# Performance work log

Hardware: AMD Instinct MI355X
Metric: run time of the kernel (lower is better)

Reference implementation:

```python
import jax, jax.numpy as jnp
import numpy as np

B, C, T = 128, 64, 16384
RED = 16  # channels // reduction_ratio

def setup_inputs() -> dict:
    key = jax.random.key(0)
    k0, k1, k2 = jax.random.split(key, 3)
    x = jax.random.normal(k0, (B, C, T), dtype=jnp.float32)
    # torch Linear init ~ U(-1/sqrt(fan_in), 1/sqrt(fan_in)); scaled normals are fine for a reference
    w1 = jax.random.normal(k1, (RED, C), dtype=jnp.float32) / np.sqrt(C)
    b1 = jnp.zeros((RED,), dtype=jnp.float32)
    w2 = jax.random.normal(k2, (C, RED), dtype=jnp.float32) / np.sqrt(RED)
    b2 = jnp.zeros((C,), dtype=jnp.float32)
    return {"x": x, "w1": w1, "b1": b1, "w2": w2, "b2": b2}

def reference(x, w1, b1, w2, b2):
    # squeeze: global average pool over time -> [B, C]
    u = jnp.mean(x, axis=-1)
    # excitation: Linear -> ReLU -> Linear -> Sigmoid (torch Linear: y = u @ W.T + b)
    h = jax.nn.relu(jnp.einsum('bc,rc->br', u, w1) + b1)
    s = jax.nn.sigmoid(jnp.einsum('br,cr->bc', h, w2) + b2)
    # channel-wise rescale
    x_recal = x * s[:, :, None]
    return (x_recal, s)
```

## Files before the change

kernel.cpp:

```cpp
#include <hip/hip_runtime.h>

#define BB 128
#define CC 64
#define TT 16384
#define RED 16
#define ROWS (BB * CC)
#define T4 (TT / 4)
#define GB 16
#define NG (BB / GB)
#define ROWS_G (GB * CC)

typedef float f4 __attribute__((ext_vector_type(4)));

__global__ __launch_bounds__(256) void se_reduce(const f4* __restrict__ x,
                                                 float* __restrict__ u,
                                                 int rowBase) {
    const int row = rowBase + blockIdx.x;
    const int tid = threadIdx.x;
    const f4* xr = x + (size_t)row * T4;

    float sum = 0.f;
#pragma unroll
    for (int k = 0; k < T4 / 256; ++k) {
        f4 v = xr[tid + k * 256];
        sum += (v.x + v.y) + (v.z + v.w);
    }
#pragma unroll
    for (int off = 32; off > 0; off >>= 1)
        sum += __shfl_down(sum, off, 64);

    __shared__ float wsum[4];
    const int lane = tid & 63, wid = tid >> 6;
    if (lane == 0) wsum[wid] = sum;
    __syncthreads();
    if (tid == 0)
        u[row] = (wsum[0] + wsum[1] + wsum[2] + wsum[3]) * (1.0f / TT);
}

__global__ __launch_bounds__(256) void se_scale(const f4* __restrict__ x,
                                                const float* __restrict__ u,
                                                const float* __restrict__ w1,
                                                const float* __restrict__ b1,
                                                const float* __restrict__ w2,
                                                const float* __restrict__ b2,
                                                f4* __restrict__ out,
                                                float* __restrict__ s_out,
                                                int rowBase) {
    const int row = rowBase + blockIdx.x;
    const int b = row >> 6;
    const int c = row & (CC - 1);
    const int tid = threadIdx.x;
    __shared__ float s_sh;

    if (tid < 64) {
        const int r = tid & 15, q = tid >> 4;
        const float* ub  = u  + b * CC + q * 16;
        const float* w1p = w1 + r * CC + q * 16;
        float p = 0.f;
#pragma unroll
        for (int j = 0; j < 16; ++j) p = fmaf(ub[j], w1p[j], p);
        p += __shfl_xor(p, 16, 64);
        p += __shfl_xor(p, 32, 64);
        const float h = fmaxf(p + b1[r], 0.f);
        float prod = h * w2[c * RED + r];
        prod += __shfl_xor(prod, 1, 64);
        prod += __shfl_xor(prod, 2, 64);
        prod += __shfl_xor(prod, 4, 64);
        prod += __shfl_xor(prod, 8, 64);
        if (tid == 0) {
            const float sv = 1.0f / (1.0f + expf(-(prod + b2[c])));
            s_sh = sv;
            s_out[row] = sv;
        }
    }
    __syncthreads();
    const float sv = s_sh;

    const f4* xr = x + (size_t)row * T4;
    f4* orow = out + (size_t)row * T4;
#pragma unroll
    for (int k = 0; k < T4 / 256; ++k) {
        f4 v = xr[tid + k * 256];
        v.x *= sv; v.y *= sv; v.z *= sv; v.w *= sv;
        __builtin_nontemporal_store(v, &orow[tid + k * 256]);
    }
}

extern "C" void kernel_launch(void* const* d_in, const int* in_sizes, int n_in,
                              void* d_out, int out_size, void* d_ws, size_t ws_size,
                              hipStream_t stream) {
    const float* x  = (const float*)d_in[0];
    const float* w1 = (const float*)d_in[1];
    const float* b1 = (const float*)d_in[2];
    const float* w2 = (const float*)d_in[3];
    const float* b2 = (const float*)d_in[4];

    float* out   = (float*)d_out;
    float* s_out = out + (size_t)ROWS * TT;
    float* u_ws  = (float*)d_ws;

    for (int g = 0; g < NG; ++g) {
        se_reduce<<<ROWS_G, 256, 0, stream>>>((const f4*)x, u_ws, g * ROWS_G);
        se_scale<<<ROWS_G, 256, 0, stream>>>((const f4*)x, u_ws, w1, b1, w2, b2,
                                             (f4*)out, s_out, g * ROWS_G);
    }
}
```

Baseline: 276.4 us.

## Fuse reduce and scale into a cooperative persistent kernel with pipelined next-group reduction

Replaces the 16 alternating reduce/scale launches with a single cooperative kernel of 512 blocks, each handling two rows per group. While scaling the current group, each block also reads the next group's rows and accumulates their means, then synchronises the whole grid before the next group's MLP. The aim is to cut launch overhead and to overlap the reduction read with the scale pass while the data is still likely in cache. The cost is grid-wide barriers, and each pass now reads two rows at once. If the cooperative launch fails, a non-cooperative path runs instead that uses the same overlapped reduction.

```diff
diff --git a/kernel.cpp b/kernel.cpp
--- a/kernel.cpp
+++ b/kernel.cpp
@@ -1,4 +1,7 @@
 #include <hip/hip_runtime.h>
+#include <hip/hip_cooperative_groups.h>
+
+namespace cg = cooperative_groups;
 
 #define BB 128
 #define CC 64
@@ -9,99 +12,203 @@
 #define GB 16
 #define NG (BB / GB)
 #define ROWS_G (GB * CC)
+#define GRID_C 512
 
 typedef float f4 __attribute__((ext_vector_type(4)));
 
-__global__ __launch_bounds__(256) void se_reduce(const f4* __restrict__ x,
-                                                 float* __restrict__ u,
-                                                 int rowBase) {
-    const int row = rowBase + blockIdx.x;
+__device__ __forceinline__ float wave_mlp(const float* __restrict__ u,
+                                          const float* __restrict__ w1,
+                                          const float* __restrict__ b1,
+                                          const float* __restrict__ w2,
+                                          const float* __restrict__ b2,
+                                          int b, int c, int lane) {
+    const int r = lane & 15, q = lane >> 4;
+    const float* ub  = u  + b * CC + q * 16;
+    const float* w1p = w1 + r * CC + q * 16;
+    float p = 0.f;
+#pragma unroll
+    for (int j = 0; j < 16; ++j) p = fmaf(ub[j], w1p[j], p);
+    p += __shfl_xor(p, 16, 64);
+    p += __shfl_xor(p, 32, 64);
+    const float h = fmaxf(p + b1[r], 0.f);
+    float prod = h * w2[c * RED + r];
+    prod += __shfl_xor(prod, 1, 64);
+    prod += __shfl_xor(prod, 2, 64);
+    prod += __shfl_xor(prod, 4, 64);
+    prod += __shfl_xor(prod, 8, 64);
+    return 1.0f / (1.0f + expf(-(prod + b2[c])));
+}
+
+__global__ __launch_bounds__(256, 2) void se_fused(
+        const f4* __restrict__ x,
+        const float* __restrict__ w1, const float* __restrict__ b1,
+        const float* __restrict__ w2, const float* __restrict__ b2,
+        f4* __restrict__ out, float* __restrict__ s_out,
+        float* __restrict__ u) {
+    cg::grid_group grid = cg::this_grid();
+    const int i = blockIdx.x;
     const int tid = threadIdx.x;
+    const int lane = tid & 63, wid = tid >> 6;
+    __shared__ float wsum[2][4];
+    __shared__ float s_sh[2];
+
+#pragma unroll
+    for (int rr = 0; rr < 2; ++rr) {
+        const f4* xr = x + (size_t)(i + rr * GRID_C) * T4;
+        float sum = 0.f;
+#pragma unroll 4
+        for (int k = 0; k < T4 / 256; ++k) {
+            f4 v = xr[tid + k * 256];
+            sum += (v.x + v.y) + (v.z + v.w);
+        }
+#pragma unroll
+        for (int off = 32; off; off >>= 1) sum += __shfl_down(sum, off, 64);
+        if (lane == 0) wsum[rr][wid] = sum;
+        __syncthreads();
+    }
+    if (tid < 2)
+        u[i + tid * GRID_C] =
+            (wsum[tid][0] + wsum[tid][1] + wsum[tid][2] + wsum[tid][3]) * (1.0f / TT);
+    grid.sync();
+
+    for (int g = 0; g < NG; ++g) {
+        const int row0 = g * ROWS_G + i;
+        if (wid < 2) {
+            const int row = row0 + wid * GRID_C;
+            const float sv = wave_mlp(u, w1, b1, w2, b2, row >> 6, row & (CC - 1), lane);
+            if (lane == 0) { s_sh[wid] = sv; s_out[row] = sv; }
+        }
+        __syncthreads();
+
+#pragma unroll
+        for (int rr = 0; rr < 2; ++rr) {
+            const int row = row0 + rr * GRID_C;
+            const float sv = s_sh[rr];
+            const f4* xr = x + (size_t)row * T4;
+            f4* orw = out + (size_t)row * T4;
+            if (g + 1 < NG) {
+                const f4* xn = x + (size_t)(row + ROWS_G) * T4;
+                float sum = 0.f;
+#pragma unroll 4
+                for (int k = 0; k < T4 / 256; ++k) {
+                    f4 v = xr[tid + k * 256];
+                    f4 w = xn[tid + k * 256];
+                    v.x *= sv; v.y *= sv; v.z *= sv; v.w *= sv;
+                    __builtin_nontemporal_store(v, &orw[tid + k * 256]);
+                    sum += (w.x + w.y) + (w.z + w.w);
+                }
+#pragma unroll
+                for (int off = 32; off; off >>= 1) sum += __shfl_down(sum, off, 64);
+                if (lane == 0) wsum[rr][wid] = sum;
+            } else {
+#pragma unroll 4
+                for (int k = 0; k < T4 / 256; ++k) {
+                    f4 v = xr[tid + k * 256];
+                    v.x *= sv; v.y *= sv; v.z *= sv; v.w *= sv;
+                    __builtin_nontemporal_store(v, &orw[tid + k * 256]);
+                }
+            }
+        }
+        if (g + 1 < NG) {
+            __syncthreads();
+            if (tid < 2)
+                u[row0 + ROWS_G + tid * GRID_C] =
+                    (wsum[tid][0] + wsum[tid][1] + wsum[tid][2] + wsum[tid][3]) * (1.0f / TT);
+            grid.sync();
+        }
+    }
+}
+
+__global__ __launch_bounds__(256) void se_reduce0(const f4* __restrict__ x,
+                                                  float* __restrict__ u) {
+    const int row = blockIdx.x;
+    const int tid = threadIdx.x;
+    const int lane = tid & 63, wid = tid >> 6;
     const f4* xr = x + (size_t)row * T4;
-
     float sum = 0.f;
-#pragma unroll
+#pragma unroll 4
     for (int k = 0; k < T4 / 256; ++k) {
         f4 v = xr[tid + k * 256];
         sum += (v.x + v.y) + (v.z + v.w);
     }
 #pragma unroll
-    for (int off = 32; off > 0; off >>= 1)
-        sum += __shfl_down(sum, off, 64);
-
+    for (int off = 32; off; off >>= 1) sum += __shfl_down(sum, off, 64);
     __shared__ float wsum[4];
-    const int lane = tid & 63, wid = tid >> 6;
     if (lane == 0) wsum[wid] = sum;
     __syncthreads();
-    if (tid == 0)
-        u[row] = (wsum[0] + wsum[1] + wsum[2] + wsum[3]) * (1.0f / TT);
-}
-
-__global__ __launch_bounds__(256) void se_scale(const f4* __restrict__ x,
-                                                const float* __restrict__ u,
-                                                const float* __restrict__ w1,
-                                                const float* __restrict__ b1,
-                                                const float* __restrict__ w2,
-                                                const float* __restrict__ b2,
-                                                f4* __restrict__ out,
-                                                float* __restrict__ s_out,
-                                                int rowBase) {
-    const int row = rowBase + blockIdx.x;
-    const int b = row >> 6;
-    const int c = row & (CC - 1);
+    if (tid == 0) u[row] = (wsum[0] + wsum[1] + wsum[2] + wsum[3]) * (1.0f / TT);
+}
+
+__global__ __launch_bounds__(256) void se_phase(
+        const f4* __restrict__ x,
+        const float* __restrict__ w1, const float* __restrict__ b1,
+        const float* __restrict__ w2, const float* __restrict__ b2,
+        f4* __restrict__ out, float* __restrict__ s_out,
+        float* __restrict__ u, int g) {
+    const int row = g * ROWS_G + blockIdx.x;
     const int tid = threadIdx.x;
+    const int lane = tid & 63, wid = tid >> 6;
+    __shared__ float wsum[4];
     __shared__ float s_sh;
 
     if (tid < 64) {
-        const int r = tid & 15, q = tid >> 4;
-        const float* ub  = u  + b * CC + q * 16;
-        const float* w1p = w1 + r * CC + q * 16;
-        float p = 0.f;
-#pragma unroll
-        for (int j = 0; j < 16; ++j) p = fmaf(ub[j], w1p[j], p);
-        p += __shfl_xor(p, 16, 64);
-        p += __shfl_xor(p, 32, 64);
-        const float h = fmaxf(p + b1[r], 0.f);
-        float prod = h * w2[c * RED + r];
-        prod += __shfl_xor(prod, 1, 64);
-        prod += __shfl_xor(prod, 2, 64);
-        prod += __shfl_xor(prod, 4, 64);
-        prod += __shfl_xor(prod, 8, 64);
-        if (tid == 0) {
-            const float sv = 1.0f / (1.0f + expf(-(prod + b2[c])));
-            s_sh = sv;
-            s_out[row] = sv;
-        }
+        const float sv = wave_mlp(u, w1, b1, w2, b2, row >> 6, row & (CC - 1), lane);
+        if (lane == 0) { s_sh = sv; s_out[row] = sv; }
     }
     __syncthreads();
     const float sv = s_sh;
 
     const f4* xr = x + (size_t)row * T4;
-    f4* orow = out + (size_t)row * T4;
-#pragma unroll
-    for (int k = 0; k < T4 / 256; ++k) {
-        f4 v = xr[tid + k * 256];
-        v.x *= sv; v.y *= sv; v.z *= sv; v.w *= sv;
-        __builtin_nontemporal_store(v, &orow[tid + k * 256]);
+    f4* orw = out + (size_t)row * T4;
+    if (g + 1 < NG) {
+        const f4* xn = x + (size_t)(row + ROWS_G) * T4;
+        float sum = 0.f;
+#pragma unroll 4
+        for (int k = 0; k < T4 / 256; ++k) {
+            f4 v = xr[tid + k * 256];
+            f4 w = xn[tid + k * 256];
+            v.x *= sv; v.y *= sv; v.z *= sv; v.w *= sv;
+            __builtin_nontemporal_store(v, &orw[tid + k * 256]);
+            sum += (w.x + w.y) + (w.z + w.w);
+        }
+#pragma unroll
+        for (int off = 32; off; off >>= 1) sum += __shfl_down(sum, off, 64);
+        if (lane == 0) wsum[wid] = sum;
+        __syncthreads();
+        if (tid == 0)
+            u[row + ROWS_G] = (wsum[0] + wsum[1] + wsum[2] + wsum[3]) * (1.0f / TT);
+    } else {
+#pragma unroll 4
+        for (int k = 0; k < T4 / 256; ++k) {
+            f4 v = xr[tid + k * 256];
+            v.x *= sv; v.y *= sv; v.z *= sv; v.w *= sv;
+            __builtin_nontemporal_store(v, &orw[tid + k * 256]);
+        }
     }
 }
 
 extern "C" void kernel_launch(void* const* d_in, const int* in_sizes, int n_in,
                               void* d_out, int out_size, void* d_ws, size_t ws_size,
                               hipStream_t stream) {
-    const float* x  = (const float*)d_in[0];
+    const f4*    x  = (const f4*)d_in[0];
     const float* w1 = (const float*)d_in[1];
     const float* b1 = (const float*)d_in[2];
     const float* w2 = (const float*)d_in[3];
     const float* b2 = (const float*)d_in[4];
 
-    float* out   = (float*)d_out;
-    float* s_out = out + (size_t)ROWS * TT;
+    f4*    out   = (f4*)d_out;
+    float* s_out = (float*)d_out + (size_t)ROWS * TT;
     float* u_ws  = (float*)d_ws;
 
-    for (int g = 0; g < NG; ++g) {
-        se_reduce<<<ROWS_G, 256, 0, stream>>>((const f4*)x, u_ws, g * ROWS_G);
-        se_scale<<<ROWS_G, 256, 0, stream>>>((const f4*)x, u_ws, w1, b1, w2, b2,
-                                             (f4*)out, s_out, g * ROWS_G);
-    }
-}
+    void* args[] = {(void*)&x, (void*)&w1, (void*)&b1, (void*)&w2, (void*)&b2,
+                    (void*)&out, (void*)&s_out, (void*)&u_ws};
+    hipError_t err = hipLaunchCooperativeKernel((const void*)se_fused,
+                                                dim3(GRID_C), dim3(256),
+                                                args, 0, stream);
+    if (err != hipSuccess) {
+        se_reduce0<<<ROWS_G, 256, 0, stream>>>(x, u_ws);
+        for (int g = 0; g < NG; ++g)
+            se_phase<<<ROWS_G, 256, 0, stream>>>(x, w1, b1, w2, b2,
+                                                 out, s_out, u_ws, g);
+    }
+}
```

Measured after the change: 744.5 us. 2.69x slower.

## Fuse next group's reduction into current group's scale kernel

Applied to the files above, without the earlier changes.

Each scale launch now also computes the channel means for the next batch group, so one launch per group replaces the separate reduce and scale pair, with a single standalone reduce for the first group. This cuts launch count and lets the reduction reads of one group run alongside the scale traffic of another, keeping the next group's data warm in cache. The reduction loops use two accumulators with partial unrolling. The trade-off is more work per block, and the chunking only pays off if the group's x slice stays resident in the cache between launches.

```diff
diff --git a/kernel.cpp b/kernel.cpp
--- a/kernel.cpp
+++ b/kernel.cpp
@@ -12,96 +12,114 @@
 
 typedef float f4 __attribute__((ext_vector_type(4)));
 
-__global__ __launch_bounds__(256) void se_reduce(const f4* __restrict__ x,
-                                                 float* __restrict__ u,
-                                                 int rowBase) {
-    const int row = rowBase + blockIdx.x;
+__device__ __forceinline__ float wave_mlp(const float* __restrict__ u,
+                                          const float* __restrict__ w1,
+                                          const float* __restrict__ b1,
+                                          const float* __restrict__ w2,
+                                          const float* __restrict__ b2,
+                                          int b, int c, int lane) {
+    const int r = lane & 15, q = lane >> 4;
+    const float* ub  = u  + b * CC + q * 16;
+    const float* w1p = w1 + r * CC + q * 16;
+    float p = 0.f;
+#pragma unroll
+    for (int j = 0; j < 16; ++j) p = fmaf(ub[j], w1p[j], p);
+    p += __shfl_xor(p, 16, 64);
+    p += __shfl_xor(p, 32, 64);
+    const float h = fmaxf(p + b1[r], 0.f);
+    float prod = h * w2[c * RED + r];
+    prod += __shfl_xor(prod, 1, 64);
+    prod += __shfl_xor(prod, 2, 64);
+    prod += __shfl_xor(prod, 4, 64);
+    prod += __shfl_xor(prod, 8, 64);
+    return 1.0f / (1.0f + expf(-(prod + b2[c])));
+}
+
+__global__ __launch_bounds__(256) void se_reduce0(const f4* __restrict__ x,
+                                                  float* __restrict__ u) {
+    const int row = blockIdx.x;
     const int tid = threadIdx.x;
+    const int lane = tid & 63, wid = tid >> 6;
     const f4* xr = x + (size_t)row * T4;
-
-    float sum = 0.f;
+    float s0 = 0.f, s1 = 0.f;
+#pragma unroll 8
+    for (int k = 0; k < T4 / 256; k += 2) {
+        f4 a = xr[tid + k * 256];
+        f4 b = xr[tid + (k + 1) * 256];
+        s0 += (a.x + a.y) + (a.z + a.w);
+        s1 += (b.x + b.y) + (b.z + b.w);
+    }
+    float sum = s0 + s1;
 #pragma unroll
-    for (int k = 0; k < T4 / 256; ++k) {
-        f4 v = xr[tid + k * 256];
-        sum += (v.x + v.y) + (v.z + v.w);
-    }
-#pragma unroll
-    for (int off = 32; off > 0; off >>= 1)
-        sum += __shfl_down(sum, off, 64);
-
+    for (int off = 32; off; off >>= 1) sum += __shfl_down(sum, off, 64);
     __shared__ float wsum[4];
-    const int lane = tid & 63, wid = tid >> 6;
     if (lane == 0) wsum[wid] = sum;
     __syncthreads();
-    if (tid == 0)
-        u[row] = (wsum[0] + wsum[1] + wsum[2] + wsum[3]) * (1.0f / TT);
+    if (tid == 0) u[row] = (wsum[0] + wsum[1] + wsum[2] + wsum[3]) * (1.0f / TT);
 }
 
-__global__ __launch_bounds__(256) void se_scale(const f4* __restrict__ x,
-                                                const float* __restrict__ u,
-                                                const float* __restrict__ w1,
-                                                const float* __restrict__ b1,
-                                                const float* __restrict__ w2,
-                                                const float* __restrict__ b2,
-                                                f4* __restrict__ out,
-                                                float* __restrict__ s_out,
-                                                int rowBase) {
-    const int row = rowBase + blockIdx.x;
-    const int b = row >> 6;
-    const int c = row & (CC - 1);
+__global__ __launch_bounds__(256) void se_phase(
+        const f4* __restrict__ x,
+        const float* __restrict__ w1, const float* __restrict__ b1,
+        const float* __restrict__ w2, const float* __restrict__ b2,
+        f4* __restrict__ out, float* __restrict__ s_out,
+        float* __restrict__ u, int g) {
+    const int row = g * ROWS_G + blockIdx.x;
     const int tid = threadIdx.x;
+    const int lane = tid & 63, wid = tid >> 6;
+    __shared__ float wsum[4];
     __shared__ float s_sh;
 
-    if (tid < 64) {
-        const int r = tid & 15, q = tid >> 4;
-        const float* ub  = u  + b * CC + q * 16;
-        const float* w1p = w1 + r * CC + q * 16;
-        float p = 0.f;
+    if (wid == 0) {
+        const float sv = wave_mlp(u, w1, b1, w2, b2, row >> 6, row & (CC - 1), lane);
+        if (lane == 0) { s_sh = sv; s_out[row] = sv; }
+    }
+
+    if (g + 1 < NG) {
+        const f4* xn = x + (size_t)(row + ROWS_G) * T4;
+        float s0 = 0.f, s1 = 0.f;
+#pragma unroll 8
+        for (int k = 0; k < T4 / 256; k += 2) {
+            f4 a = xn[tid + k * 256];
+            f4 b = xn[tid + (k + 1) * 256];
+            s0 += (a.x + a.y) + (a.z + a.w);
+            s1 += (b.x + b.y) + (b.z + b.w);
+        }
+        float sum = s0 + s1;
 #pragma unroll
-        for (int j = 0; j < 16; ++j) p = fmaf(ub[j], w1p[j], p);
-        p += __shfl_xor(p, 16, 64);
-        p += __shfl_xor(p, 32, 64);
-        const float h = fmaxf(p + b1[r], 0.f);
-        float prod = h * w2[c * RED + r];
-        prod += __shfl_xor(prod, 1, 64);
-        prod += __shfl_xor(prod, 2, 64);
-        prod += __shfl_xor(prod, 4, 64);
-        prod += __shfl_xor(prod, 8, 64);
-        if (tid == 0) {
-            const float sv = 1.0f / (1.0f + expf(-(prod + b2[c])));
-            s_sh = sv;
-            s_out[row] = sv;
-        }
+        for (int off = 32; off; off >>= 1) sum += __shfl_down(sum, off, 64);
+        if (lane == 0) wsum[wid] = sum;
     }
     __syncthreads();
+    if (g + 1 < NG && tid == 0)
+        u[row + ROWS_G] = (wsum[0] + wsum[1] + wsum[2] + wsum[3]) * (1.0f / TT);
+
     const float sv = s_sh;
-
     const f4* xr = x + (size_t)row * T4;
-    f4* orow = out + (size_t)row * T4;
-#pragma unroll
+    f4* orw = out + (size_t)row * T4;
+#pragma unroll 8
     for (int k = 0; k < T4 / 256; ++k) {
         f4 v = xr[tid + k * 256];
         v.x *= sv; v.y *= sv; v.z *= sv; v.w *= sv;
-        __builtin_nontemporal_store(v, &orow[tid + k * 256]);
+        __builtin_nontemporal_store(v, &orw[tid + k * 256]);
     }
 }
 
 extern "C" void kernel_launch(void* const* d_in, const int* in_sizes, int n_in,
                               void* d_out, int out_size, void* d_ws, size_t ws_size,
                               hipStream_t stream) {
-    const float* x  = (const float*)d_in[0];
+    const f4*    x  = (const f4*)d_in[0];
     const float* w1 = (const float*)d_in[1];
     const float* b1 = (const float*)d_in[2];
     const float* w2 = (const float*)d_in[3];
     const float* b2 = (const float*)d_in[4];
 
-    float* out   = (float*)d_out;
-    float* s_out = out + (size_t)ROWS * TT;
+    f4*    out   = (f4*)d_out;
+    float* s_out = (float*)d_out + (size_t)ROWS * TT;
     float* u_ws  = (float*)d_ws;
 
-    for (int g = 0; g < NG; ++g) {
-        se_reduce<<<ROWS_G, 256, 0, stream>>>((const f4*)x, u_ws, g * ROWS_G);
-        se_scale<<<ROWS_G, 256, 0, stream>>>((const f4*)x, u_ws, w1, b1, w2, b2,
-                                             (f4*)out, s_out, g * ROWS_G);
-    }
+    se_reduce0<<<ROWS_G, 256, 0, stream>>>(x, u_ws);
+    for (int g = 0; g < NG; ++g)
+        se_phase<<<ROWS_G, 256, 0, stream>>>(x, w1, b1, w2, b2,
+                                             out, s_out, u_ws, g);
 }
```

Result: faster. 265.5 us (median of 2 runs) (-3.9%).
